# Kernel optimization log

Hardware: AMD Instinct MI355X
Metric: run time of the kernel (lower is better)

## Reference

```python
import jax, jax.numpy as jnp
import numpy as np
from jax import lax

T, B, I, H = 32768, 1, 128, 512  # seq_len, batch(=1 due to squeeze(1)), input_dim, hidden_dim
HEAD = 25

def setup_inputs() -> dict:
    key = jax.random.key(0)
    ks = jax.random.split(key, 8)
    s = 1.0 / np.sqrt(H)  # pytorch LSTM init scale
    return {
        "x": jax.random.normal(ks[0], (T, B, I), dtype=jnp.float32),
        "W_ih": jax.random.uniform(ks[1], (4 * H, I), jnp.float32, -s, s),
        "W_hh": jax.random.uniform(ks[2], (4 * H, H), jnp.float32, -s, s),
        "b_ih": jax.random.uniform(ks[3], (4 * H,), jnp.float32, -s, s),
        "b_hh": jax.random.uniform(ks[4], (4 * H,), jnp.float32, -s, s),
        "W1": jax.random.uniform(ks[5], (HEAD, H), jnp.float32, -s, s),
        "b1": jax.random.uniform(ks[6], (HEAD,), jnp.float32, -s, s),
        "Wout": jax.random.uniform(ks[7], (1, HEAD), jnp.float32, -s, s),
    }

def reference(x, W_ih, W_hh, b_ih, b_hh, W1, b1, Wout):
    # Precompute input projections for all timesteps (one big GEMM): [T, B, 4H]
    xg = jnp.einsum('tbi,gi->tbg', x, W_ih) + (b_ih + b_hh)

    def step(carry, xg_t):
        h, c = carry  # [B, H] each
        gates = xg_t + h @ W_hh.T  # [B, 4H]
        i_g, f_g, g_g, o_g = jnp.split(gates, 4, axis=-1)  # pytorch gate order i,f,g,o
        i = jax.nn.sigmoid(i_g)
        f = jax.nn.sigmoid(f_g)
        g = jnp.tanh(g_g)
        o = jax.nn.sigmoid(o_g)
        c = f * c + i * g
        h = o * jnp.tanh(c)
        return (h, c), h

    h0 = jnp.zeros((B, H), x.dtype)
    _, hs = lax.scan(step, (h0, h0), xg)  # hs: [T, B, H]

    hid = hs[:, 0, :]  # h_1.squeeze(1) -> [T, H]
    # forward applies c1 then out (c2 is defined but unused in the original)
    out = (hid @ W1.T + b1) @ Wout.T  # [T, 1]
    return out
```

## Files before the change

### kernel.cpp

```cpp
#include <hip/hip_runtime.h>
#include <math.h>


#define T_SEQ 32768
#define HID   512
#define INP   128
#define NWG   32
#define GRID  256
#define NTH   512
#define HSL   16
#define KW    64
#define KX    16
#define NPK   256

typedef unsigned long long u64;
typedef unsigned int u32;

__device__ __forceinline__ float fast_sigmoid(float x) {
    return 1.0f / (1.0f + __expf(-x));
}
__device__ __forceinline__ float fast_tanh(float x) {
    float a = fabsf(x);
    float e = __expf(-2.0f * a);
    float r = (1.0f - e) / (1.0f + e);
    return copysignf(r, x);
}

__device__ __forceinline__ void wg_barrier_lgkm() {
    __builtin_amdgcn_sched_barrier(0);
    asm volatile("s_waitcnt lgkmcnt(0)" ::: "memory");
    __builtin_amdgcn_s_barrier();
    __builtin_amdgcn_sched_barrier(0);
}

__global__ void __launch_bounds__(NTH, 1) lstm_persist(
    const float* __restrict__ x,
    const float* __restrict__ W_ih,
    const float* __restrict__ W_hh,
    const float* __restrict__ b_ih,
    const float* __restrict__ b_hh,
    const float* __restrict__ W1,
    const float* __restrict__ b1,
    const float* __restrict__ Wout,
    u64* __restrict__ hb_fast,
    u64* __restrict__ hb_slow,
    float* __restrict__ out)
{
    const int bid = blockIdx.x;
    if (bid & 7) return;
    const int w   = bid >> 3;
    const int tid = threadIdx.x;
    const int wv  = tid >> 6;
    const int l   = tid & 63;
    const int rw  = l >> 3;
    const int j   = l & 7;
    const int g   = rw >> 1;
    const int b   = rw & 1;
    const bool is_out = (w == 0 && wv == 1);

    __shared__ __align__(16) float h_lds[2][HID];
    __shared__ u64 gather_lds[8];

    const int grow = g * HID + w * HSL + 2 * wv + b;

    float wr[KW], wi[KX];
#pragma unroll
    for (int kk = 0; kk < 16; ++kk) {
        const int p = (kk + 2 * j) & 15;
        const float4 v4 = *(const float4*)&W_hh[grow * HID + j * KW + 4 * p];
        wr[4 * kk + 0] = v4.x; wr[4 * kk + 1] = v4.y;
        wr[4 * kk + 2] = v4.z; wr[4 * kk + 3] = v4.w;
    }
#pragma unroll
    for (int k = 0; k < KX; k += 4) {
        const float4 v4 = *(const float4*)&W_ih[grow * INP + j * KX + k];
        wi[k] = v4.x; wi[k + 1] = v4.y; wi[k + 2] = v4.z; wi[k + 3] = v4.w;
    }
    float brow = b_ih[grow] + b_hh[grow];

    float weff_o[8];
    float be = 0.0f;
#pragma unroll
    for (int i = 0; i < 8; ++i) weff_o[i] = 0.0f;
    if (is_out) {
#pragma unroll
        for (int i = 0; i < 8; ++i) {
            float s = 0.0f;
            for (int p = 0; p < 25; ++p) s += Wout[p] * W1[p * HID + l + 64 * i];
            weff_o[i] = s;
        }
        for (int p = 0; p < 25; ++p) be += b1[p] * Wout[p];
    }
#pragma unroll
    for (int k = 0; k < KW; ++k) asm volatile("" : "+v"(wr[k]));
#pragma unroll
    for (int k = 0; k < KX; ++k) asm volatile("" : "+v"(wi[k]));
#pragma unroll
    for (int i = 0; i < 8; ++i) asm volatile("" : "+v"(weff_o[i]));
    asm volatile("" : "+v"(brow));
    asm volatile("" : "+v"(be));

    float c = 0.0f;
    float xa[KX];
#pragma unroll
    for (int k = 0; k < KX; ++k) xa[k] = x[j * KX + k];

    bool dead = false;
    bool slowMode = false;
    int  slowSteps = 0;

    for (u32 t = 0; t <= T_SEQ; ++t) {
        if (t == T_SEQ && w != 0) break;

        float xd0 = 0.0f, xd1 = 0.0f, xd2 = 0.0f, xd3 = 0.0f;
#pragma unroll
        for (int k = 0; k < KX; k += 4) {
            xd0 += wi[k + 0] * xa[k + 0];
            xd1 += wi[k + 1] * xa[k + 1];
            xd2 += wi[k + 2] * xa[k + 2];
            xd3 += wi[k + 3] * xa[k + 3];
        }
        const int tn = (t + 1 < T_SEQ) ? (int)(t + 1) : (T_SEQ - 1);
        if (wv != 0) {
#pragma unroll
            for (int k = 0; k < KX; k += 4) {
                const float4 x4 = *(const float4*)&x[tn * INP + j * KX + k];
                xa[k + 0] = x4.x; xa[k + 1] = x4.y;
                xa[k + 2] = x4.z; xa[k + 3] = x4.w;
            }
        }

        if (wv == 0 && !dead) {
            float2* HL = (float2*)h_lds[t & 1];
            if (t == 0) {
                float2 z; z.x = 0.0f; z.y = 0.0f;
                HL[l +   0] = z;
                HL[l +  64] = z;
                HL[l + 128] = z;
                HL[l + 192] = z;
            } else {
                const int par = (t & 1) * NPK;
                const u64 a0 = (u64)(hb_fast + par + l);
                const u64 a1 = a0 +  64u * sizeof(u64);
                const u64 a2 = a0 + 128u * sizeof(u64);
                const u64 a3 = a0 + 192u * sizeof(u64);
                const u64* PS = hb_slow + par;
                const u32 tLo = t & 15u;
                const u32 tHi = (t >> 4) & 15u;
                const int ft = (t < 4) ? 8192 : 512;
                bool mine = false;
                bool slow = slowMode;
                int it = 0;
                while (true) {
                    if (!mine) {
                        u64 p0, p1, p2, p3;
                        if (!slow) {
                            asm volatile(
                                "global_load_dwordx2 %0, %4, off sc0\n\t"
                                "global_load_dwordx2 %1, %5, off sc0\n\t"
                                "global_load_dwordx2 %2, %6, off sc0\n\t"
                                "global_load_dwordx2 %3, %7, off sc0\n\t"
                                "s_waitcnt vmcnt(0)"
                                : "=&v"(p0), "=&v"(p1), "=&v"(p2), "=&v"(p3)
                                : "v"(a0), "v"(a1), "v"(a2), "v"(a3)
                                : "memory");
                            __builtin_amdgcn_sched_barrier(0);
                        } else {
                            p0 = __hip_atomic_load(PS + l, __ATOMIC_RELAXED,
                                                   __HIP_MEMORY_SCOPE_AGENT);
                            p1 = __hip_atomic_load(PS + l + 64, __ATOMIC_RELAXED,
                                                   __HIP_MEMORY_SCOPE_AGENT);
                            p2 = __hip_atomic_load(PS + l + 128, __ATOMIC_RELAXED,
                                                   __HIP_MEMORY_SCOPE_AGENT);
                            p3 = __hip_atomic_load(PS + l + 192, __ATOMIC_RELAXED,
                                                   __HIP_MEMORY_SCOPE_AGENT);
                        }
                        const bool ok =
                            ((((u32)p0 ^ tLo) & 15u) == 0u) &&
                            ((((u32)(p0 >> 32) ^ tHi) & 15u) == 0u) &&
                            ((((u32)p1 ^ tLo) & 15u) == 0u) &&
                            ((((u32)(p1 >> 32) ^ tHi) & 15u) == 0u) &&
                            ((((u32)p2 ^ tLo) & 15u) == 0u) &&
                            ((((u32)(p2 >> 32) ^ tHi) & 15u) == 0u) &&
                            ((((u32)p3 ^ tLo) & 15u) == 0u) &&
                            ((((u32)(p3 >> 32) ^ tHi) & 15u) == 0u);
                        if (ok) {
                            float2 h0, h1, h2, h3;
                            h0.x = __uint_as_float((u32)p0);
                            h0.y = __uint_as_float((u32)(p0 >> 32));
                            h1.x = __uint_as_float((u32)p1);
                            h1.y = __uint_as_float((u32)(p1 >> 32));
                            h2.x = __uint_as_float((u32)p2);
                            h2.y = __uint_as_float((u32)(p2 >> 32));
                            h3.x = __uint_as_float((u32)p3);
                            h3.y = __uint_as_float((u32)(p3 >> 32));
                            HL[l +   0] = h0;
                            HL[l +  64] = h1;
                            HL[l + 128] = h2;
                            HL[l + 192] = h3;
                            mine = true;
                        }
                    }
                    if (__ballot(mine) == ~0ull) break;
                    ++it;
                    if (it == ft) slow = true;
                    if (it > (1 << 22)) { dead = true; break; }
                }
                if (slow && !slowMode && t >= 4) {
                    if (++slowSteps >= 8) slowMode = true;
                }
            }
        }

        wg_barrier_lgkm();

        if (t < T_SEQ) {
            float a0 = xd0, a1 = xd1, a2 = xd2, a3 = xd3;
            const float4* hl4 = (const float4*)&h_lds[t & 1][j * KW];
#pragma unroll
            for (int kk = 0; kk < 16; ++kk) {
                const int p = (kk + 2 * j) & 15;
                const float4 h4 = hl4[p];
                a0 += wr[4 * kk + 0] * h4.x;
                a1 += wr[4 * kk + 1] * h4.y;
                a2 += wr[4 * kk + 2] * h4.z;
                a3 += wr[4 * kk + 3] * h4.w;
            }
            if (wv == 0) {
#pragma unroll
                for (int k = 0; k < KX; k += 4) {
                    const float4 x4 = *(const float4*)&x[tn * INP + j * KX + k];
                    xa[k + 0] = x4.x; xa[k + 1] = x4.y;
                    xa[k + 2] = x4.z; xa[k + 3] = x4.w;
                }
            }
            float acc = (a0 + a1) + (a2 + a3);
            acc += __shfl_xor(acc, 1);
            acc += __shfl_xor(acc, 2);
            acc += __shfl_xor(acc, 4);
            acc += brow;
            const float ig = acc;
            const float fg = __shfl(acc, l + 16);
            const float gg = __shfl(acc, l + 32);
            const float og = __shfl(acc, l + 48);
            const float iv = fast_sigmoid(ig);
            const float fv = fast_sigmoid(fg);
            const float gv = fast_tanh(gg);
            const float ov = fast_sigmoid(og);
            c = fv * c + iv * gv;
            const float hv = ov * fast_tanh(c);
            const float hv1 = __shfl(hv, 8);
            if (l == 0) {
                const u32 b0  = (__float_as_uint(hv)  & ~15u) | ((t + 1) & 15u);
                const u32 b1v = (__float_as_uint(hv1) & ~15u) | (((t + 1) >> 4) & 15u);
                gather_lds[wv] = ((u64)b1v << 32) | (u64)b0;
            }

            wg_barrier_lgkm();

            const int mwv = 1 + (int)(t % 7u);
            if (wv == 0 && l < 8) {
                const u64 pkt = gather_lds[l];
                const u64 adf = (u64)&hb_fast[((t + 1) & 1) * NPK + w * 8 + l];
                asm volatile("global_store_dwordx2 %0, %1, off"
                             :: "v"(adf), "v"(pkt) : "memory");
            } else if (wv == mwv && l < 8) {
                const u64 pkt = gather_lds[l];
                __hip_atomic_store(&hb_slow[((t + 1) & 1) * NPK + w * 8 + l],
                                   pkt, __ATOMIC_RELAXED,
                                   __HIP_MEMORY_SCOPE_AGENT);
            }
        }

        if (is_out && t >= 1) {
            float pd = 0.0f;
#pragma unroll
            for (int i = 0; i < 8; ++i)
                pd += h_lds[t & 1][l + 64 * i] * weff_o[i];
            pd += __shfl_xor(pd, 1);
            pd += __shfl_xor(pd, 2);
            pd += __shfl_xor(pd, 4);
            pd += __shfl_xor(pd, 8);
            pd += __shfl_xor(pd, 16);
            pd += __shfl_xor(pd, 32);
            if (l == 0) out[t - 1] = pd + be;
        }
    }
}

extern "C" void kernel_launch(void* const* d_in, const int* in_sizes, int n_in,
                              void* d_out, int out_size, void* d_ws, size_t ws_size,
                              hipStream_t stream)
{
    const float* x    = (const float*)d_in[0];
    const float* W_ih = (const float*)d_in[1];
    const float* W_hh = (const float*)d_in[2];
    const float* b_ih = (const float*)d_in[3];
    const float* b_hh = (const float*)d_in[4];
    const float* W1   = (const float*)d_in[5];
    const float* b1   = (const float*)d_in[6];
    const float* Wout = (const float*)d_in[7];
    float* out = (float*)d_out;

    u64* hb_fast = (u64*)d_ws;
    u64* hb_slow = hb_fast + 2 * NPK;

    hipMemsetAsync(d_ws, 0, 4 * NPK * sizeof(u64), stream);
    lstm_persist<<<GRID, NTH, 0, stream>>>(x, W_ih, W_hh, b_ih, b_hh, W1, b1,
                                           Wout, hb_fast, hb_slow, out);
}
```

Measured before the change: 76.80 ms.

## Simplify h exchange to single atomic buffer and stage x through LDS

Drops the dual fast/slow hidden-state exchange (non-coherent sc0 loads plus a fallback atomic buffer) in favour of one buffer read and written with agent-scope relaxed atomics. It launches exactly 32 workgroups instead of 256 with early exits. The x input projection for wave 0 is now read from a double-buffered LDS slot filled by wave 1, which prefetches x two steps ahead, taking global x loads off the critical path of the polling wave. The cost is that every poll now goes through the coherent atomic path instead of possibly faster non-coherent loads, and there is extra LDS traffic each step.

```diff
diff --git a/kernel.cpp b/kernel.cpp
--- a/kernel.cpp
+++ b/kernel.cpp
@@ -6,7 +6,6 @@
 #define HID   512
 #define INP   128
 #define NWG   32
-#define GRID  256
 #define NTH   512
 #define HSL   16
 #define KW    64
@@ -42,13 +41,10 @@
     const float* __restrict__ W1,
     const float* __restrict__ b1,
     const float* __restrict__ Wout,
-    u64* __restrict__ hb_fast,
-    u64* __restrict__ hb_slow,
+    u64* __restrict__ hbuf,
     float* __restrict__ out)
 {
-    const int bid = blockIdx.x;
-    if (bid & 7) return;
-    const int w   = bid >> 3;
+    const int w   = blockIdx.x;
     const int tid = threadIdx.x;
     const int wv  = tid >> 6;
     const int l   = tid & 63;
@@ -56,9 +52,10 @@
     const int j   = l & 7;
     const int g   = rw >> 1;
     const int b   = rw & 1;
-    const bool is_out = (w == 0 && wv == 1);
+    const bool is_out = (w == 0 && wv == 2);
 
     __shared__ __align__(16) float h_lds[2][HID];
+    __shared__ __align__(16) float x_lds[2][INP];
     __shared__ u64 gather_lds[8];
 
     const int grow = g * HID + w * HSL + 2 * wv + b;
@@ -101,32 +98,44 @@
     asm volatile("" : "+v"(be));
 
     float c = 0.0f;
-    float xa[KX];
+    float xa[KX], xn[KX];
 #pragma unroll
     for (int k = 0; k < KX; ++k) xa[k] = x[j * KX + k];
+#pragma unroll
+    for (int k = 0; k < KX; ++k) xn[k] = x[INP + j * KX + k];
+
+    if (wv == 1 && l < 8) {
+        float4* xp = (float4*)&x_lds[0][j * KX];
+        float4 v;
+        v.x = xa[0];  v.y = xa[1];  v.z = xa[2];  v.w = xa[3];  xp[0] = v;
+        v.x = xa[4];  v.y = xa[5];  v.z = xa[6];  v.w = xa[7];  xp[1] = v;
+        v.x = xa[8];  v.y = xa[9];  v.z = xa[10]; v.w = xa[11]; xp[2] = v;
+        v.x = xa[12]; v.y = xa[13]; v.z = xa[14]; v.w = xa[15]; xp[3] = v;
+    }
+    __syncthreads();
 
     bool dead = false;
-    bool slowMode = false;
-    int  slowSteps = 0;
 
     for (u32 t = 0; t <= T_SEQ; ++t) {
         if (t == T_SEQ && w != 0) break;
 
         float xd0 = 0.0f, xd1 = 0.0f, xd2 = 0.0f, xd3 = 0.0f;
-#pragma unroll
-        for (int k = 0; k < KX; k += 4) {
-            xd0 += wi[k + 0] * xa[k + 0];
-            xd1 += wi[k + 1] * xa[k + 1];
-            xd2 += wi[k + 2] * xa[k + 2];
-            xd3 += wi[k + 3] * xa[k + 3];
-        }
-        const int tn = (t + 1 < T_SEQ) ? (int)(t + 1) : (T_SEQ - 1);
         if (wv != 0) {
 #pragma unroll
             for (int k = 0; k < KX; k += 4) {
-                const float4 x4 = *(const float4*)&x[tn * INP + j * KX + k];
-                xa[k + 0] = x4.x; xa[k + 1] = x4.y;
-                xa[k + 2] = x4.z; xa[k + 3] = x4.w;
+                xd0 += wi[k + 0] * xa[k + 0];
+                xd1 += wi[k + 1] * xa[k + 1];
+                xd2 += wi[k + 2] * xa[k + 2];
+                xd3 += wi[k + 3] * xa[k + 3];
+            }
+#pragma unroll
+            for (int k = 0; k < KX; ++k) xa[k] = xn[k];
+            const int tn2 = (t + 2 < T_SEQ) ? (int)(t + 2) : (T_SEQ - 1);
+#pragma unroll
+            for (int k = 0; k < KX; k += 4) {
+                const float4 x4 = *(const float4*)&x[tn2 * INP + j * KX + k];
+                xn[k + 0] = x4.x; xn[k + 1] = x4.y;
+                xn[k + 2] = x4.z; xn[k + 3] = x4.w;
             }
         }
 
@@ -139,42 +148,22 @@
                 HL[l + 128] = z;
                 HL[l + 192] = z;
             } else {
-                const int par = (t & 1) * NPK;
-                const u64 a0 = (u64)(hb_fast + par + l);
-                const u64 a1 = a0 +  64u * sizeof(u64);
-                const u64 a2 = a0 + 128u * sizeof(u64);
-                const u64 a3 = a0 + 192u * sizeof(u64);
-                const u64* PS = hb_slow + par;
+                const u64* P = hbuf + (t & 1) * NPK;
                 const u32 tLo = t & 15u;
                 const u32 tHi = (t >> 4) & 15u;
-                const int ft = (t < 4) ? 8192 : 512;
                 bool mine = false;
-                bool slow = slowMode;
-                int it = 0;
+                int guard = 0;
                 while (true) {
                     if (!mine) {
                         u64 p0, p1, p2, p3;
-                        if (!slow) {
-                            asm volatile(
-                                "global_load_dwordx2 %0, %4, off sc0\n\t"
-                                "global_load_dwordx2 %1, %5, off sc0\n\t"
-                                "global_load_dwordx2 %2, %6, off sc0\n\t"
-                                "global_load_dwordx2 %3, %7, off sc0\n\t"
-                                "s_waitcnt vmcnt(0)"
-                                : "=&v"(p0), "=&v"(p1), "=&v"(p2), "=&v"(p3)
-                                : "v"(a0), "v"(a1), "v"(a2), "v"(a3)
-                                : "memory");
-                            __builtin_amdgcn_sched_barrier(0);
-                        } else {
-                            p0 = __hip_atomic_load(PS + l, __ATOMIC_RELAXED,
-                                                   __HIP_MEMORY_SCOPE_AGENT);
-                            p1 = __hip_atomic_load(PS + l + 64, __ATOMIC_RELAXED,
-                                                   __HIP_MEMORY_SCOPE_AGENT);
-                            p2 = __hip_atomic_load(PS + l + 128, __ATOMIC_RELAXED,
-                                                   __HIP_MEMORY_SCOPE_AGENT);
-                            p3 = __hip_atomic_load(PS + l + 192, __ATOMIC_RELAXED,
-                                                   __HIP_MEMORY_SCOPE_AGENT);
-                        }
+                        p0 = __hip_atomic_load(P + l, __ATOMIC_RELAXED,
+                                               __HIP_MEMORY_SCOPE_AGENT);
+                        p1 = __hip_atomic_load(P + l + 64, __ATOMIC_RELAXED,
+                                               __HIP_MEMORY_SCOPE_AGENT);
+                        p2 = __hip_atomic_load(P + l + 128, __ATOMIC_RELAXED,
+                                               __HIP_MEMORY_SCOPE_AGENT);
+                        p3 = __hip_atomic_load(P + l + 192, __ATOMIC_RELAXED,
+                                               __HIP_MEMORY_SCOPE_AGENT);
                         const bool ok =
                             ((((u32)p0 ^ tLo) & 15u) == 0u) &&
                             ((((u32)(p0 >> 32) ^ tHi) & 15u) == 0u) &&
@@ -202,19 +191,26 @@
                         }
                     }
                     if (__ballot(mine) == ~0ull) break;
-                    ++it;
-                    if (it == ft) slow = true;
-                    if (it > (1 << 22)) { dead = true; break; }
+                    if (++guard > (1 << 22)) { dead = true; break; }
                 }
-                if (slow && !slowMode && t >= 4) {
-                    if (++slowSteps >= 8) slowMode = true;
-                }
             }
         }
 
         wg_barrier_lgkm();
 
         if (t < T_SEQ) {
+            if (wv == 0) {
+                const float4* xl4 = (const float4*)&x_lds[t & 1][j * KX];
+                const float4 xv0 = xl4[0];
+                const float4 xv1 = xl4[1];
+                const float4 xv2 = xl4[2];
+                const float4 xv3 = xl4[3];
+                xd0 = wi[0] * xv0.x + wi[4] * xv1.x + wi[8]  * xv2.x + wi[12] * xv3.x;
+                xd1 = wi[1] * xv0.y + wi[5] * xv1.y + wi[9]  * xv2.y + wi[13] * xv3.y;
+                xd2 = wi[2] * xv0.z + wi[6] * xv1.z + wi[10] * xv2.z + wi[14] * xv3.z;
+                xd3 = wi[3] * xv0.w + wi[7] * xv1.w + wi[11] * xv2.w + wi[15] * xv3.w;
+            }
+
             float a0 = xd0, a1 = xd1, a2 = xd2, a3 = xd3;
             const float4* hl4 = (const float4*)&h_lds[t & 1][j * KW];
 #pragma unroll
@@ -225,14 +221,6 @@
                 a1 += wr[4 * kk + 1] * h4.y;
                 a2 += wr[4 * kk + 2] * h4.z;
                 a3 += wr[4 * kk + 3] * h4.w;
-            }
-            if (wv == 0) {
-#pragma unroll
-                for (int k = 0; k < KX; k += 4) {
-                    const float4 x4 = *(const float4*)&x[tn * INP + j * KX + k];
-                    xa[k + 0] = x4.x; xa[k + 1] = x4.y;
-                    xa[k + 2] = x4.z; xa[k + 3] = x4.w;
-                }
             }
             float acc = (a0 + a1) + (a2 + a3);
             acc += __shfl_xor(acc, 1);
@@ -255,18 +243,21 @@
                 const u32 b1v = (__float_as_uint(hv1) & ~15u) | (((t + 1) >> 4) & 15u);
                 gather_lds[wv] = ((u64)b1v << 32) | (u64)b0;
             }
+            if (wv == 1 && l < 8) {
+                float4* xp = (float4*)&x_lds[(t + 1) & 1][j * KX];
+                float4 v;
+                v.x = xa[0];  v.y = xa[1];  v.z = xa[2];  v.w = xa[3];  xp[0] = v;
+                v.x = xa[4];  v.y = xa[5];  v.z = xa[6];  v.w = xa[7];  xp[1] = v;
+                v.x = xa[8];  v.y = xa[9];  v.z = xa[10]; v.w = xa[11]; xp[2] = v;
+                v.x = xa[12]; v.y = xa[13]; v.z = xa[14]; v.w = xa[15]; xp[3] = v;
+            }
 
             wg_barrier_lgkm();
 
             const int mwv = 1 + (int)(t % 7u);
-            if (wv == 0 && l < 8) {
+            if (wv == mwv && l < 8) {
                 const u64 pkt = gather_lds[l];
-                const u64 adf = (u64)&hb_fast[((t + 1) & 1) * NPK + w * 8 + l];
-                asm volatile("global_store_dwordx2 %0, %1, off"
-                             :: "v"(adf), "v"(pkt) : "memory");
-            } else if (wv == mwv && l < 8) {
-                const u64 pkt = gather_lds[l];
-                __hip_atomic_store(&hb_slow[((t + 1) & 1) * NPK + w * 8 + l],
+                __hip_atomic_store(&hbuf[((t + 1) & 1) * NPK + w * 8 + l],
                                    pkt, __ATOMIC_RELAXED,
                                    __HIP_MEMORY_SCOPE_AGENT);
             }
@@ -302,10 +293,9 @@
     const float* Wout = (const float*)d_in[7];
     float* out = (float*)d_out;
 
-    u64* hb_fast = (u64*)d_ws;
-    u64* hb_slow = hb_fast + 2 * NPK;
-
-    hipMemsetAsync(d_ws, 0, 4 * NPK * sizeof(u64), stream);
-    lstm_persist<<<GRID, NTH, 0, stream>>>(x, W_ih, W_hh, b_ih, b_hh, W1, b1,
-                                           Wout, hb_fast, hb_slow, out);
-}
+    u64* hbuf = (u64*)d_ws;
+
+    hipMemsetAsync(d_ws, 0, 2 * NPK * sizeof(u64), stream);
+    lstm_persist<<<NWG, NTH, 0, stream>>>(x, W_ih, W_hh, b_ih, b_hh, W1, b1,
+                                          Wout, hbuf, out);
+}
```

New measurement: 76.27 ms. Within noise of the previous version (-0.7%).
